# Kernel tuning notes

Measured on AMD Instinct MI355X. Metric: run time of the kernel, lower is better.

The kernel has to match this reference:

```python
import jax, jax.numpy as jnp
import numpy as np

D_MODEL = 2048
N_HEADS = 16
HEAD_DIM = D_MODEL // N_HEADS


def setup_inputs() -> dict:
    key = jax.random.key(0)
    ks = jax.random.split(key, 5)
    b, l, d = 2, 2048, D_MODEL
    x = jax.random.normal(ks[0], (b, l, d), dtype=jnp.float32)
    # torch nn.Linear weights: y = x @ W.T + b, W shape [out, in]
    s_qkv = 1.0 / np.sqrt(d)
    W_qkv = jax.random.uniform(ks[1], (3 * d, d), dtype=jnp.float32, minval=-s_qkv, maxval=s_qkv)
    b_qkv = jax.random.uniform(ks[2], (3 * d,), dtype=jnp.float32, minval=-s_qkv, maxval=s_qkv)
    W_out = jax.random.uniform(ks[3], (d, d), dtype=jnp.float32, minval=-s_qkv, maxval=s_qkv)
    b_out = jax.random.uniform(ks[4], (d,), dtype=jnp.float32, minval=-s_qkv, maxval=s_qkv)
    return {"x": x, "W_qkv": W_qkv, "b_qkv": b_qkv, "W_out": W_out, "b_out": b_out}


def reference(x, W_qkv, b_qkv, W_out, b_out):
    b, l, d = x.shape
    h, e = N_HEADS, HEAD_DIM
    qkv = x @ W_qkv.T + b_qkv                      # [b, l, 3d]
    q, k, v = jnp.split(qkv, 3, axis=-1)
    # split heads: [b, l, h, e]
    q = q.reshape(b, l, h, e)
    k = k.reshape(b, l, h, e)
    v = v.reshape(b, l, h, e)
    scale = 1.0 / jnp.sqrt(jnp.float32(e))
    scores = jnp.einsum('bqhe,bkhe->bhqk', q, k) * scale  # [b, h, l, l]
    # causal mask (is_causal=True)
    causal = jnp.tril(jnp.ones((l, l), dtype=bool))
    scores = jnp.where(causal[None, None], scores, -jnp.inf)
    attn = jax.nn.softmax(scores, axis=-1)          # dropout p=0 -> identity
    out = jnp.einsum('bhqk,bkhe->bqhe', attn, v)    # [b, l, h, e]
    out = out.reshape(b, l, d)                      # merge heads
    out = out @ W_out.T + b_out
    return out
```

## Files before the change

kernel.cpp:

```cpp
#include <hip/hip_runtime.h>
#include <hip/hip_bf16.h>

#define B_ 2
#define L_ 2048
#define D_ 2048
#define H_ 16
#define E_ 128
#define M_ 4096
#define K_ 2048
#define N3_ 6144

typedef __attribute__((ext_vector_type(4))) float f32x4;
typedef short s16x8 __attribute__((ext_vector_type(8)));

__device__ inline void gld_lds16(const void* g, void* l) {
    __builtin_amdgcn_global_load_lds(
        (const __attribute__((address_space(1))) void*)g,
        (__attribute__((address_space(3))) void*)l, 16, 0, 0);
}

__global__ __launch_bounds__(256)
void cast_bf16(const float* __restrict__ in, __hip_bfloat16* __restrict__ out, int n8)
{
    const int i = blockIdx.x * 256 + threadIdx.x;
    if (i >= n8) return;
    const float4 a = ((const float4*)in)[2 * i];
    const float4 b = ((const float4*)in)[2 * i + 1];
    union { __hip_bfloat16 h[8]; uint4 u; } o;
    o.h[0] = __float2bfloat16(a.x); o.h[1] = __float2bfloat16(a.y);
    o.h[2] = __float2bfloat16(a.z); o.h[3] = __float2bfloat16(a.w);
    o.h[4] = __float2bfloat16(b.x); o.h[5] = __float2bfloat16(b.y);
    o.h[6] = __float2bfloat16(b.z); o.h[7] = __float2bfloat16(b.w);
    ((uint4*)out)[i] = o.u;
}

__global__ __launch_bounds__(256)
void gemm_bf16_nt(const __hip_bfloat16* __restrict__ A,
                  const __hip_bfloat16* __restrict__ W,
                  const float* __restrict__ bias,
                  __hip_bfloat16* __restrict__ q,
                  __hip_bfloat16* __restrict__ k,
                  __hip_bfloat16* __restrict__ vT,
                  float* __restrict__ o,
                  const int mode)
{
    __shared__ __hip_bfloat16 As[128 * 32];
    __shared__ __hip_bfloat16 Bs[128 * 32];

    const int t    = threadIdx.x;
    const int lane = t & 63;
    const int w    = t >> 6;
    const int l15  = lane & 15;
    const int hi   = lane >> 4;
    const int wr   = w >> 1, wc = w & 1;
    const int m0   = blockIdx.y << 7;
    const int n0   = blockIdx.x << 7;

    f32x4 acc[4][4];
    const f32x4 z4 = {0.f, 0.f, 0.f, 0.f};
    #pragma unroll
    for (int m = 0; m < 4; ++m)
        #pragma unroll
        for (int n = 0; n < 4; ++n) acc[m][n] = z4;

    const __hip_bfloat16* Ab = A + (size_t)m0 * K_;
    const __hip_bfloat16* Bb = W + (size_t)n0 * K_;
    const int srow = t >> 2;
    const int sc   = (t & 3) << 3;

    for (int k0 = 0; k0 < K_; k0 += 32) {
        #pragma unroll
        for (int j = 0; j < 2; ++j) {
            gld_lds16(Ab + (size_t)(j * 64 + srow) * K_ + k0 + sc,
                      (char*)As + j * 4096 + w * 1024);
            gld_lds16(Bb + (size_t)(j * 64 + srow) * K_ + k0 + sc,
                      (char*)Bs + j * 4096 + w * 1024);
        }
        __syncthreads();
        s16x8 af[4], bf[4];
        #pragma unroll
        for (int m = 0; m < 4; ++m)
            af[m] = *(const s16x8*)(As + (wr * 64 + m * 16 + l15) * 32 + hi * 8);
        #pragma unroll
        for (int n = 0; n < 4; ++n)
            bf[n] = *(const s16x8*)(Bs + (wc * 64 + n * 16 + l15) * 32 + hi * 8);
        #pragma unroll
        for (int m = 0; m < 4; ++m)
            #pragma unroll
            for (int n = 0; n < 4; ++n)
                acc[m][n] = __builtin_amdgcn_mfma_f32_16x16x32_bf16(af[m], bf[n], acc[m][n], 0, 0, 0);
        __syncthreads();
    }

    if (mode == 1) {
        #pragma unroll
        for (int n = 0; n < 4; ++n) {
            const int col = n0 + wc * 64 + n * 16 + l15;
            const float bn = bias[col];
            #pragma unroll
            for (int m = 0; m < 4; ++m) {
                const int rowb = m0 + wr * 64 + m * 16 + hi * 4;
                #pragma unroll
                for (int i = 0; i < 4; ++i)
                    o[(size_t)(rowb + i) * D_ + col] = acc[m][n][i] + bn;
            }
        }
    } else {
        const int which = n0 >> 11;
        const int h     = (n0 >> 7) & 15;
        #pragma unroll
        for (int n = 0; n < 4; ++n) {
            const int e  = wc * 64 + n * 16 + l15;
            const float bn = bias[n0 + e];
            #pragma unroll
            for (int m = 0; m < 4; ++m) {
                const int rowb = m0 + wr * 64 + m * 16 + hi * 4;
                #pragma unroll
                for (int i = 0; i < 4; ++i) {
                    const int mm = rowb + i;
                    const int b  = mm >> 11;
                    const int l  = mm & 2047;
                    const __hip_bfloat16 val = __float2bfloat16(acc[m][n][i] + bn);
                    if (which == 0)
                        q[((size_t)((b * H_ + h) * L_ + l) << 7) + e] = val;
                    else if (which == 1)
                        k[((size_t)((b * H_ + h) * L_ + l) << 7) + e] = val;
                    else
                        vT[(((size_t)(b * H_ + h) << 7) + e) * L_ + l] = val;
                }
            }
        }
    }
}

__global__ __launch_bounds__(256)
void attn_mfma(const __hip_bfloat16* __restrict__ Qg,
               const __hip_bfloat16* __restrict__ Kg,
               const __hip_bfloat16* __restrict__ vTg,
               __hip_bfloat16* __restrict__ O)
{
    __shared__ __hip_bfloat16 Ks[2][64 * 128];
    __shared__ __hip_bfloat16 Vt[2][128 * 64];
    __shared__ __hip_bfloat16 Ps[4 * 1024];

    const int t    = threadIdx.x;
    const int lane = t & 63;
    const int w    = t >> 6;
    const int l15  = lane & 15;
    const int hi   = lane >> 4;
    const int pq   = blockIdx.x;
    const int bh   = blockIdx.y;
    const size_t base = (size_t)bh * (L_ * E_);
    const float scale = 0.08838834764831843f;
    const int krow = t >> 4;
    const int kc16 = t & 15;

    const __hip_bfloat16* Kbh  = Kg  + base;
    const __hip_bfloat16* vTbh = vTg + base;

    auto stage = [&](int kt2, int buf) {
        const __hip_bfloat16* Kb = Kbh + ((size_t)(kt2 << 6)) * E_;
        char* kd = (char*)Ks + buf * 16384 + (w << 10);
        #pragma unroll
        for (int j = 0; j < 4; ++j) {
            const int row = (j << 4) + krow;
            const int csw = kc16 ^ (row & 7);
            gld_lds16(Kb + (size_t)row * E_ + (csw << 3), kd + (j << 12));
        }
        const __hip_bfloat16* Vb = vTbh + (kt2 << 6);
        char* vd = (char*)Vt + buf * 16384 + (w << 10);
        #pragma unroll
        for (int j = 0; j < 4; ++j) {
            const int e  = (j << 5) + (t >> 3);
            const int g8 = (t & 7) ^ (e & 7);
            gld_lds16(Vb + (size_t)e * L_ + (g8 << 3), vd + (j << 12));
        }
    };

    const f32x4 z4 = {0.f, 0.f, 0.f, 0.f};

    #pragma unroll 1
    for (int seg = 0; seg < 2; ++seg) {
        const int qt = seg ? pq : 31 - pq;
        const int q0 = (qt << 6) + (w << 4);

        s16x8 qf[4];
        #pragma unroll
        for (int e0 = 0; e0 < 4; ++e0)
            qf[e0] = *(const s16x8*)(Qg + base + (size_t)(q0 + l15) * E_ + e0 * 32 + hi * 8);

        f32x4 oacc[8];
        #pragma unroll
        for (int ef = 0; ef < 8; ++ef) oacc[ef] = z4;
        float mrow[4] = {-1e30f, -1e30f, -1e30f, -1e30f};
        float lrow[4] = {0.f, 0.f, 0.f, 0.f};

        stage(0, 0);
        __syncthreads();

        for (int kt = 0; kt <= qt; ++kt) {
            const int cur = kt & 1;
            if (kt < qt) stage(kt + 1, cur ^ 1);

            const char* Ksc = (const char*)Ks + cur * 16384;
            const char* Vtc = (const char*)Vt + cur * 16384;

            f32x4 sf[4];
            #pragma unroll
            for (int c = 0; c < 4; ++c) {
                f32x4 s = z4;
                const int row = (c << 4) + l15;
                #pragma unroll
                for (int e0 = 0; e0 < 4; ++e0) {
                    const int ch = ((e0 << 2) + hi) ^ (row & 7);
                    const s16x8 kf = *(const s16x8*)(Ksc + (row << 8) + (ch << 4));
                    s = __builtin_amdgcn_mfma_f32_16x16x32_bf16(qf[e0], kf, s, 0, 0, 0);
                }
                sf[c] = s;
            }

            float p4[4][4];
            float tmax[4] = {-1e30f, -1e30f, -1e30f, -1e30f};
            if (kt == qt) {
                const int qg = q0 + (hi << 2);
                #pragma unroll
                for (int c = 0; c < 4; ++c) {
                    const int kvg = (kt << 6) + (c << 4) + l15;
                    #pragma unroll
                    for (int i = 0; i < 4; ++i) {
                        float s = sf[c][i] * scale;
                        if (kvg > qg + i) s = -1e30f;
                        p4[c][i] = s;
                        tmax[i] = fmaxf(tmax[i], s);
                    }
                }
            } else {
                #pragma unroll
                for (int c = 0; c < 4; ++c)
                    #pragma unroll
                    for (int i = 0; i < 4; ++i) {
                        const float s = sf[c][i] * scale;
                        p4[c][i] = s;
                        tmax[i] = fmaxf(tmax[i], s);
                    }
            }
            float fsc[4];
            #pragma unroll
            for (int i = 0; i < 4; ++i) {
                float v = tmax[i];
                v = fmaxf(v, __shfl_xor(v, 1));
                v = fmaxf(v, __shfl_xor(v, 2));
                v = fmaxf(v, __shfl_xor(v, 4));
                v = fmaxf(v, __shfl_xor(v, 8));
                const float mnew = fmaxf(mrow[i], v);
                fsc[i] = __expf(mrow[i] - mnew);
                mrow[i] = mnew;
                float sum = 0.f;
                #pragma unroll
                for (int c = 0; c < 4; ++c) {
                    const float pe = __expf(p4[c][i] - mnew);
                    p4[c][i] = pe;
                    sum += pe;
                }
                sum += __shfl_xor(sum, 1);
                sum += __shfl_xor(sum, 2);
                sum += __shfl_xor(sum, 4);
                sum += __shfl_xor(sum, 8);
                lrow[i] = lrow[i] * fsc[i] + sum;
            }
            #pragma unroll
            for (int ef = 0; ef < 8; ++ef)
                #pragma unroll
                for (int i = 0; i < 4; ++i) oacc[ef][i] *= fsc[i];

            #pragma unroll
            for (int c = 0; c < 4; ++c)
                #pragma unroll
                for (int i = 0; i < 4; ++i) {
                    const int r   = (hi << 2) + i;
                    const int col = (c << 4) + l15;
                    const int ch  = (col >> 3) ^ (r & 7);
                    const int by  = (r << 7) + ((ch << 4) | ((col & 7) << 1));
                    *(__hip_bfloat16*)((char*)Ps + (w << 11) + by) = __float2bfloat16(p4[c][i]);
                }
            asm volatile("s_waitcnt lgkmcnt(0)" ::: "memory");

            #pragma unroll
            for (int kh = 0; kh < 2; ++kh) {
                const int chp = ((kh << 2) + hi) ^ (l15 & 7);
                const s16x8 pa = *(const s16x8*)((char*)Ps + (w << 11) + (l15 << 7) + (chp << 4));
                #pragma unroll
                for (int ef = 0; ef < 8; ++ef) {
                    const int e   = (ef << 4) + l15;
                    const int chv = ((kh << 2) + hi) ^ (e & 7);
                    const s16x8 vb = *(const s16x8*)(Vtc + (e << 7) + (chv << 4));
                    oacc[ef] = __builtin_amdgcn_mfma_f32_16x16x32_bf16(pa, vb, oacc[ef], 0, 0, 0);
                }
            }
            __syncthreads();
        }

        const int b = bh >> 4, h = bh & 15;
        float invl[4];
        #pragma unroll
        for (int i = 0; i < 4; ++i) invl[i] = 1.f / lrow[i];
        #pragma unroll
        for (int ef = 0; ef < 8; ++ef) {
            const int e = (ef << 4) + l15;
            #pragma unroll
            for (int i = 0; i < 4; ++i) {
                const int row = q0 + (hi << 2) + i;
                O[((size_t)(b * L_ + row) * D_) + (h << 7) + e] =
                    __float2bfloat16(oacc[ef][i] * invl[i]);
            }
        }
    }
}

extern "C" void kernel_launch(void* const* d_in, const int* in_sizes, int n_in,
                              void* d_out, int out_size, void* d_ws, size_t ws_size,
                              hipStream_t stream)
{
    const float* x    = (const float*)d_in[0];
    const float* Wqkv = (const float*)d_in[1];
    const float* bqkv = (const float*)d_in[2];
    const float* Wout = (const float*)d_in[3];
    const float* bout = (const float*)d_in[4];
    float* out = (float*)d_out;

    __hip_bfloat16* xb  = (__hip_bfloat16*)d_ws;
    __hip_bfloat16* wqb = xb  + (size_t)M_ * K_;
    __hip_bfloat16* wob = wqb + (size_t)N3_ * K_;
    __hip_bfloat16* qb  = wob + (size_t)D_ * K_;
    __hip_bfloat16* kb  = qb  + (size_t)M_ * D_;
    __hip_bfloat16* vtb = kb  + (size_t)M_ * D_;
    __hip_bfloat16* aob = vtb + (size_t)M_ * D_;

    cast_bf16<<<(M_ * K_ / 8) / 256, 256, 0, stream>>>(x, xb, M_ * K_ / 8);
    cast_bf16<<<(N3_ * K_ / 8) / 256, 256, 0, stream>>>(Wqkv, wqb, N3_ * K_ / 8);
    cast_bf16<<<(D_ * K_ / 8) / 256, 256, 0, stream>>>(Wout, wob, D_ * K_ / 8);

    dim3 blk(256);
    dim3 g1(N3_ / 128, M_ / 128);
    gemm_bf16_nt<<<g1, blk, 0, stream>>>(xb, wqb, bqkv, qb, kb, vtb, nullptr, 0);

    dim3 g2(16, B_ * H_);
    attn_mfma<<<g2, blk, 0, stream>>>(qb, kb, vtb, aob);

    dim3 g3(D_ / 128, M_ / 128);
    gemm_bf16_nt<<<g3, blk, 0, stream>>>(aob, wob, bout, nullptr, nullptr, nullptr, out, 1);
}
```

Baseline: 447.0 us.

## Add 256x256-tile 8-wave QKV GEMM with phased double-buffered LDS pipeline

Replaces the QKV projection GEMM with a new kernel that uses 256x256 tiles, 512 threads, and a 64-deep K step. Global-to-LDS loads go into a double-buffered, XOR-swizzled 128KB LDS region and are split into four phases interleaved with MFMA groups, with barriers between phases and s_setprio raised around the math. The goal is to hide global load latency, raise data reuse per tile and avoid LDS bank conflicts. In exchange, the grid shrinks to 384 blocks, register pressure and LDS footprint are much higher, and the general GEMM is reduced to the output-projection path only.

```diff
diff --git a/kernel.cpp b/kernel.cpp
--- a/kernel.cpp
+++ b/kernel.cpp
@@ -34,15 +34,173 @@
     ((uint4*)out)[i] = o.u;
 }
 
+__global__ __launch_bounds__(512, 2)
+void gemm_qkv_8ph(const __hip_bfloat16* __restrict__ A,
+                  const __hip_bfloat16* __restrict__ W,
+                  const float* __restrict__ bias,
+                  __hip_bfloat16* __restrict__ q,
+                  __hip_bfloat16* __restrict__ k,
+                  __hip_bfloat16* __restrict__ vT)
+{
+    __shared__ char lds[131072];
+
+    const int t    = threadIdx.x;
+    const int lane = t & 63;
+    const int w    = t >> 6;
+    const int l15  = lane & 15;
+    const int hi   = lane >> 4;
+    const int wr   = w >> 2;
+    const int wc   = w & 3;
+    const int n0   = blockIdx.x << 8;
+    const int m0   = blockIdx.y << 8;
+
+    f32x4 acc[8][4];
+    const f32x4 z4 = {0.f, 0.f, 0.f, 0.f};
+    #pragma unroll
+    for (int m = 0; m < 8; ++m)
+        #pragma unroll
+        for (int n = 0; n < 4; ++n) acc[m][n] = z4;
+    s16x8 afr[4][2], bfr[4][2];
+
+    const __hip_bfloat16* Abase = A + (size_t)m0 * K_;
+    const __hip_bfloat16* Wbase = W + (size_t)n0 * K_;
+
+    auto stage_half = [&](const __hip_bfloat16* src, char* dst) {
+        #pragma unroll
+        for (int i = 0; i < 2; ++i) {
+            const int slot = (i << 9) + t;
+            const int row  = slot >> 3;
+            const int csw  = (slot & 7) ^ (row & 7);
+            gld_lds16(src + (size_t)row * K_ + (csw << 3),
+                      dst + (i << 13) + (w << 10));
+        }
+    };
+
+    stage_half(Abase,                     lds);
+    stage_half(Abase + (size_t)128 * K_,  lds + 16384);
+    stage_half(Wbase,                     lds + 32768);
+    stage_half(Wbase + (size_t)128 * K_,  lds + 49152);
+    __syncthreads();
+
+    const int NT = K_ / 64;
+    for (int T = 0; T < NT; ++T) {
+        const int  cur = T & 1;
+        const char* Al = lds + cur * 65536;
+        const char* Bl = Al + 32768;
+        char*       An = lds + (cur ^ 1) * 65536;
+        char*       Bn = An + 32768;
+        const __hip_bfloat16* Asrc = Abase + (size_t)(T + 1) * 64;
+        const __hip_bfloat16* Wsrc = Wbase + (size_t)(T + 1) * 64;
+        const bool pf = (T + 1 < NT);
+
+        auto lda = [&](int m, int kk) {
+            const int row = (wr << 7) + (m << 4) + l15;
+            const int ch  = ((kk << 2) + hi) ^ (row & 7);
+            return *(const s16x8*)(Al + row * 128 + (ch << 4));
+        };
+        auto ldb = [&](int n, int kk) {
+            const int row = (wc << 6) + (n << 4) + l15;
+            const int ch  = ((kk << 2) + hi) ^ (row & 7);
+            return *(const s16x8*)(Bl + row * 128 + (ch << 4));
+        };
+
+        #pragma unroll
+        for (int m = 0; m < 4; ++m) { afr[m][0] = lda(m, 0); afr[m][1] = lda(m, 1); }
+        #pragma unroll
+        for (int n = 0; n < 2; ++n) { bfr[n][0] = ldb(n, 0); bfr[n][1] = ldb(n, 1); }
+        if (pf) stage_half(Asrc, An);
+        __builtin_amdgcn_s_barrier();
+        __builtin_amdgcn_s_setprio(1);
+        #pragma unroll
+        for (int kk = 0; kk < 2; ++kk)
+            #pragma unroll
+            for (int n = 0; n < 2; ++n)
+                #pragma unroll
+                for (int m = 0; m < 4; ++m)
+                    acc[m][n] = __builtin_amdgcn_mfma_f32_16x16x32_bf16(
+                        afr[m][kk], bfr[n][kk], acc[m][n], 0, 0, 0);
+        __builtin_amdgcn_s_setprio(0);
+        __builtin_amdgcn_s_barrier();
+
+        #pragma unroll
+        for (int n = 0; n < 2; ++n) { bfr[2 + n][0] = ldb(2 + n, 0); bfr[2 + n][1] = ldb(2 + n, 1); }
+        if (pf) stage_half(Asrc + (size_t)128 * K_, An + 16384);
+        __builtin_amdgcn_s_barrier();
+        __builtin_amdgcn_s_setprio(1);
+        #pragma unroll
+        for (int kk = 0; kk < 2; ++kk)
+            #pragma unroll
+            for (int n = 0; n < 2; ++n)
+                #pragma unroll
+                for (int m = 0; m < 4; ++m)
+                    acc[m][2 + n] = __builtin_amdgcn_mfma_f32_16x16x32_bf16(
+                        afr[m][kk], bfr[2 + n][kk], acc[m][2 + n], 0, 0, 0);
+        __builtin_amdgcn_s_setprio(0);
+        __builtin_amdgcn_s_barrier();
+
+        #pragma unroll
+        for (int m = 0; m < 4; ++m) { afr[m][0] = lda(4 + m, 0); afr[m][1] = lda(4 + m, 1); }
+        if (pf) stage_half(Wsrc, Bn);
+        __builtin_amdgcn_s_barrier();
+        __builtin_amdgcn_s_setprio(1);
+        #pragma unroll
+        for (int kk = 0; kk < 2; ++kk)
+            #pragma unroll
+            for (int n = 0; n < 2; ++n)
+                #pragma unroll
+                for (int m = 0; m < 4; ++m)
+                    acc[4 + m][2 + n] = __builtin_amdgcn_mfma_f32_16x16x32_bf16(
+                        afr[m][kk], bfr[2 + n][kk], acc[4 + m][2 + n], 0, 0, 0);
+        __builtin_amdgcn_s_setprio(0);
+        __builtin_amdgcn_s_barrier();
+
+        if (pf) stage_half(Wsrc + (size_t)128 * K_, Bn + 16384);
+        __builtin_amdgcn_s_barrier();
+        __builtin_amdgcn_s_setprio(1);
+        #pragma unroll
+        for (int kk = 0; kk < 2; ++kk)
+            #pragma unroll
+            for (int n = 0; n < 2; ++n)
+                #pragma unroll
+                for (int m = 0; m < 4; ++m)
+                    acc[4 + m][n] = __builtin_amdgcn_mfma_f32_16x16x32_bf16(
+                        afr[m][kk], bfr[n][kk], acc[4 + m][n], 0, 0, 0);
+        __builtin_amdgcn_s_setprio(0);
+        __syncthreads();
+    }
+
+    #pragma unroll
+    for (int n = 0; n < 4; ++n) {
+        const int col   = n0 + (wc << 6) + (n << 4) + l15;
+        const int which = col >> 11;
+        const int h     = (col >> 7) & 15;
+        const int e     = col & 127;
+        const float bn  = bias[col];
+        #pragma unroll
+        for (int m = 0; m < 8; ++m) {
+            const int rowb = m0 + (wr << 7) + (m << 4) + (hi << 2);
+            #pragma unroll
+            for (int i = 0; i < 4; ++i) {
+                const int mm = rowb + i;
+                const int b  = mm >> 11;
+                const int l  = mm & 2047;
+                const __hip_bfloat16 val = __float2bfloat16(acc[m][n][i] + bn);
+                if (which == 0)
+                    q[((size_t)((b * H_ + h) * L_ + l) << 7) + e] = val;
+                else if (which == 1)
+                    k[((size_t)((b * H_ + h) * L_ + l) << 7) + e] = val;
+                else
+                    vT[(((size_t)(b * H_ + h) << 7) + e) * L_ + l] = val;
+            }
+        }
+    }
+}
+
 __global__ __launch_bounds__(256)
 void gemm_bf16_nt(const __hip_bfloat16* __restrict__ A,
                   const __hip_bfloat16* __restrict__ W,
                   const float* __restrict__ bias,
-                  __hip_bfloat16* __restrict__ q,
-                  __hip_bfloat16* __restrict__ k,
-                  __hip_bfloat16* __restrict__ vT,
-                  float* __restrict__ o,
-                  const int mode)
+                  float* __restrict__ o)
 {
     __shared__ __hip_bfloat16 As[128 * 32];
     __shared__ __hip_bfloat16 Bs[128 * 32];
@@ -92,43 +250,16 @@
         __syncthreads();
     }
 
-    if (mode == 1) {
-        #pragma unroll
-        for (int n = 0; n < 4; ++n) {
-            const int col = n0 + wc * 64 + n * 16 + l15;
-            const float bn = bias[col];
-            #pragma unroll
-            for (int m = 0; m < 4; ++m) {
-                const int rowb = m0 + wr * 64 + m * 16 + hi * 4;
-                #pragma unroll
-                for (int i = 0; i < 4; ++i)
-                    o[(size_t)(rowb + i) * D_ + col] = acc[m][n][i] + bn;
-            }
-        }
-    } else {
-        const int which = n0 >> 11;
-        const int h     = (n0 >> 7) & 15;
-        #pragma unroll
-        for (int n = 0; n < 4; ++n) {
-            const int e  = wc * 64 + n * 16 + l15;
-            const float bn = bias[n0 + e];
-            #pragma unroll
-            for (int m = 0; m < 4; ++m) {
-                const int rowb = m0 + wr * 64 + m * 16 + hi * 4;
-                #pragma unroll
-                for (int i = 0; i < 4; ++i) {
-                    const int mm = rowb + i;
-                    const int b  = mm >> 11;
-                    const int l  = mm & 2047;
-                    const __hip_bfloat16 val = __float2bfloat16(acc[m][n][i] + bn);
-                    if (which == 0)
-                        q[((size_t)((b * H_ + h) * L_ + l) << 7) + e] = val;
-                    else if (which == 1)
-                        k[((size_t)((b * H_ + h) * L_ + l) << 7) + e] = val;
-                    else
-                        vT[(((size_t)(b * H_ + h) << 7) + e) * L_ + l] = val;
-                }
-            }
+    #pragma unroll
+    for (int n = 0; n < 4; ++n) {
+        const int col = n0 + wc * 64 + n * 16 + l15;
+        const float bn = bias[col];
+        #pragma unroll
+        for (int m = 0; m < 4; ++m) {
+            const int rowb = m0 + wr * 64 + m * 16 + hi * 4;
+            #pragma unroll
+            for (int i = 0; i < 4; ++i)
+                o[(size_t)(rowb + i) * D_ + col] = acc[m][n][i] + bn;
         }
     }
 }
@@ -340,13 +471,12 @@
     cast_bf16<<<(N3_ * K_ / 8) / 256, 256, 0, stream>>>(Wqkv, wqb, N3_ * K_ / 8);
     cast_bf16<<<(D_ * K_ / 8) / 256, 256, 0, stream>>>(Wout, wob, D_ * K_ / 8);
 
-    dim3 blk(256);
-    dim3 g1(N3_ / 128, M_ / 128);
-    gemm_bf16_nt<<<g1, blk, 0, stream>>>(xb, wqb, bqkv, qb, kb, vtb, nullptr, 0);
+    dim3 g1(N3_ / 256, M_ / 256);
+    gemm_qkv_8ph<<<g1, dim3(512), 0, stream>>>(xb, wqb, bqkv, qb, kb, vtb);
 
     dim3 g2(16, B_ * H_);
-    attn_mfma<<<g2, blk, 0, stream>>>(qb, kb, vtb, aob);
+    attn_mfma<<<g2, dim3(256), 0, stream>>>(qb, kb, vtb, aob);
 
     dim3 g3(D_ / 128, M_ / 128);
-    gemm_bf16_nt<<<g3, blk, 0, stream>>>(aob, wob, bout, nullptr, nullptr, nullptr, out, 1);
-}
+    gemm_bf16_nt<<<g3, dim3(256), 0, stream>>>(aob, wob, bout, out);
+}
```

New measurement: 427.4 us. 1.05x faster.
